# Kernel optimization log

Hardware: AMD Instinct MI355X
Metric: run time of the kernel (lower is better)

## Reference

```python
import jax, jax.numpy as jnp
import numpy as np

B = 64            # batch
C = 23            # chromosomes
E = 1024          # embedding_dim (eos)
D = 1024          # d_model
BOT = 128         # bottleneck_dim (embedding table width)
BINS = 8192       # bins per chromosome (num_bins_list entries)
NUM_BINS = C * BINS
S = 3             # num_states


def setup_inputs() -> dict:
    key = jax.random.key(0)
    ks = jax.random.split(key, 7)
    eos_emb = jax.random.normal(ks[0], (B, C, E), dtype=jnp.float32)
    # embedding table: indices used are 1..NUM_BINS (cum starts at 1), so NUM_BINS+2 rows
    emb_table = jax.random.normal(ks[1], (NUM_BINS + 2, BOT), dtype=jnp.float32) * 0.02
    Wb = jax.random.normal(ks[2], (D, BOT), dtype=jnp.float32) * 0.02   # bin_projection (no bias)
    We = jax.random.normal(ks[3], (D, E), dtype=jnp.float32) * 0.02     # eos_projection weight
    be = jax.random.normal(ks[4], (D,), dtype=jnp.float32) * 0.02       # eos_projection bias
    Wfc = jax.random.normal(ks[5], (S, 2 * D), dtype=jnp.float32) * 0.02  # fc weight
    bfc = jax.random.normal(ks[6], (S,), dtype=jnp.float32) * 0.02        # fc bias
    return {"eos_emb": eos_emb, "emb_table": emb_table, "Wb": Wb,
            "We": We, "be": be, "Wfc": Wfc, "bfc": bfc}


def reference(eos_emb, emb_table, Wb, We, be, Wfc, bfc):
    # eos_projection (use_eos_proj=True): [B, C, E] -> [B, C, D]
    eos = jnp.einsum('bce,de->bcd', eos_emb, We) + be
    # embedding lookup for all bins: indices 1..NUM_BINS (contiguous across chromosomes)
    idx = 1 + jnp.arange(NUM_BINS)
    # bin_projection (bottleneck_dim != d_model): [NUM_BINS, BOT] -> [NUM_BINS, D]
    bin_emb = jnp.einsum('nk,dk->nd', emb_table[idx], Wb).reshape(C, BINS, D)
    # fc on concat([bin_emb, eos]) == bin_emb @ W1^T + eos @ W2^T + b (avoids materializing concat)
    W1, W2 = Wfc[:, :D], Wfc[:, D:]
    part_bin = jnp.einsum('cnd,sd->cns', bin_emb, W1)   # [C, BINS, S]
    part_eos = jnp.einsum('bcd,sd->bcs', eos, W2)        # [B, C, S]
    # original returns list of 23 tensors [B, BINS, S]; stacked here as [B, C, BINS, S]
    out = jax.nn.relu(part_bin[None] + part_eos[:, :, None, :] + bfc)
    return out
```

## Files before the change

kernel.cpp:

```cpp
#include <hip/hip_runtime.h>

#define B_    64
#define C_    23
#define E_    1024
#define D_    1024
#define BOT_  128
#define BINS_ 8192
#define S_    3
#define NUMBINS (C_*BINS_)

typedef float f32x4 __attribute__((ext_vector_type(4)));

#define WS_M  0
#define WS_N  512
#define WS_C0 3584
#define WS_PE 3600

__global__ __launch_bounds__(256) void kprep(const float* __restrict__ Wb,
                                             const float* __restrict__ We,
                                             const float* __restrict__ be,
                                             const float* __restrict__ Wfc,
                                             const float* __restrict__ bfc,
                                             float* __restrict__ ws) {
    const int bx = blockIdx.x;
    const int t  = threadIdx.x;

    if (bx == 96 + 12) {
        int wave = t >> 6, lane = t & 63;
        if (wave < 3) {
            const float* w2 = Wfc + wave * 2 * D_ + D_;
            float acc = 0.f;
            #pragma unroll
            for (int j = 0; j < D_ / 64; j++) {
                int d = lane + j * 64;
                acc += w2[d] * be[d];
            }
            #pragma unroll
            for (int off = 32; off; off >>= 1) acc += __shfl_down(acc, off);
            if (lane == 0) ws[WS_C0 + wave] = acc + bfc[wave];
        }
        return;
    }

    __shared__ float wv[1024];
    __shared__ float red[256];

    const int og   = t & 31;
    const int dgrp = t >> 5;

    const float* src;
    const float* wrow;
    int ostride, obase;
    float* dst;

    if (bx < 96) {
        int s = bx >> 5, e0 = (bx & 31) * 32;
        src = We; ostride = E_; obase = e0;
        wrow = Wfc + s * 2 * D_ + D_;
        dst = ws + WS_N + s * E_ + e0;
    } else {
        int m = bx - 96;
        int s = m >> 2, k0 = (m & 3) * 32;
        src = Wb; ostride = BOT_; obase = k0;
        wrow = Wfc + s * 2 * D_;
        dst = ws + WS_M + s * BOT_ + k0;
    }

    for (int i = t; i < 1024; i += 256) wv[i] = wrow[i];
    __syncthreads();

    const float* p = src + (size_t)(dgrp * 128) * ostride + obase + og;
    const float* w = wv + dgrp * 128;
    float acc = 0.f;
    #pragma unroll 8
    for (int i = 0; i < 128; i++) {
        acc += w[i] * p[(size_t)i * ostride];
    }
    red[t] = acc;
    #pragma unroll
    for (int off = 128; off >= 32; off >>= 1) {
        __syncthreads();
        if (t < off) red[t] += red[t + off];
    }
    if (t < 32) dst[t] = red[t];
}

__global__ __launch_bounds__(256) void kpe(const float* __restrict__ eos,
                                           float* ws) {
    int wave = threadIdx.x >> 6;
    int lane = threadIdx.x & 63;
    int row  = blockIdx.x * 4 + wave;
    const float* x  = eos + (size_t)row * E_;
    const float* N0 = ws + WS_N;
    float a0 = 0.f, a1 = 0.f, a2 = 0.f;
    #pragma unroll
    for (int j = 0; j < E_ / 64; j++) {
        int i = lane + j * 64;
        float v = x[i];
        a0 += v * N0[i];
        a1 += v * N0[1024 + i];
        a2 += v * N0[2048 + i];
    }
    #pragma unroll
    for (int off = 32; off; off >>= 1) {
        a0 += __shfl_down(a0, off);
        a1 += __shfl_down(a1, off);
        a2 += __shfl_down(a2, off);
    }
    if (lane == 0) {
        float* pe = ws + WS_PE + row * 3;
        pe[0] = a0 + ws[WS_C0 + 0];
        pe[1] = a1 + ws[WS_C0 + 1];
        pe[2] = a2 + ws[WS_C0 + 2];
    }
}

__global__ __launch_bounds__(256) void kmain(const float* __restrict__ table,
                                             const float* __restrict__ ws,
                                             float* __restrict__ out) {
    const int t  = threadIdx.x;
    const int c  = blockIdx.y;
    const int n0 = blockIdx.x * 256;

    __shared__ float Ml[384];
    __shared__ float pbl[768];
    __shared__ float pel[192];

    for (int i = t; i < 384; i += 256) Ml[i] = ws[WS_M + i];
    if (t < 192) {
        int b = t / 3, s = t - b * 3;
        pel[t] = ws[WS_PE + (b * C_ + c) * 3 + s];
    }
    __syncthreads();

    const f32x4* row = (const f32x4*)(table + (size_t)(1 + c * BINS_ + n0 + t) * BOT_);
    float a0 = 0.f, a1 = 0.f, a2 = 0.f;
    #pragma unroll 8
    for (int k4 = 0; k4 < 32; k4++) {
        f32x4 v = row[k4];
        int k = k4 * 4;
        a0 += v.x * Ml[k]       + v.y * Ml[k + 1]   + v.z * Ml[k + 2]   + v.w * Ml[k + 3];
        a1 += v.x * Ml[128 + k] + v.y * Ml[129 + k] + v.z * Ml[130 + k] + v.w * Ml[131 + k];
        a2 += v.x * Ml[256 + k] + v.y * Ml[257 + k] + v.z * Ml[258 + k] + v.w * Ml[259 + k];
    }
    pbl[t * 3 + 0] = a0;
    pbl[t * 3 + 1] = a1;
    pbl[t * 3 + 2] = a2;
    __syncthreads();

    if (t < 192) {
        f32x4 pv = *(const f32x4*)&pbl[t * 4];
        int s0 = t % 3;
        int s1 = (s0 + 1 == 3) ? 0 : s0 + 1;
        int s2 = (s1 + 1 == 3) ? 0 : s1 + 1;
        for (int b = 0; b < B_; b++) {
            const float* pe = &pel[b * 3];
            f32x4 o;
            o.x = fmaxf(pv.x + pe[s0], 0.f);
            o.y = fmaxf(pv.y + pe[s1], 0.f);
            o.z = fmaxf(pv.z + pe[s2], 0.f);
            o.w = fmaxf(pv.w + pe[s0], 0.f);
            f32x4* dst = (f32x4*)(out + ((size_t)(b * C_ + c) * BINS_ + n0) * 3) + t;
            __builtin_nontemporal_store(o, dst);
        }
    }
}

extern "C" void kernel_launch(void* const* d_in, const int* in_sizes, int n_in,
                              void* d_out, int out_size, void* d_ws, size_t ws_size,
                              hipStream_t stream) {
    const float* eos   = (const float*)d_in[0];
    const float* table = (const float*)d_in[1];
    const float* Wb    = (const float*)d_in[2];
    const float* We    = (const float*)d_in[3];
    const float* be    = (const float*)d_in[4];
    const float* Wfc   = (const float*)d_in[5];
    const float* bfc   = (const float*)d_in[6];
    float* out = (float*)d_out;
    float* ws  = (float*)d_ws;

    kprep<<<109, 256, 0, stream>>>(Wb, We, be, Wfc, bfc, ws);
    kpe<<<368, 256, 0, stream>>>(eos, ws);
    dim3 g(32, 23);
    kmain<<<g, 256, 0, stream>>>(table, ws, out);
}
```

Measured before the change: 59.24 us.

## Restructure kernels: merge bin projection with eos dot, split output broadcast

The prep kernel now computes all three state rows per block, reading each We/Wb column once instead of three times, so it launches 37 blocks instead of 109. The bin-table projection moves into a middle kernel that also runs the per-(b,c) eos dot products in the same launch. The middle kernel parks part_bin in the batch-0 slice of the output, and a final kernel reads it back and broadcasts across the batch. This lets the heavy table read overlap the eos work, at the cost of an extra global round-trip for part_bin and a third launch that stays dependent.

```diff
diff --git a/kernel.cpp b/kernel.cpp
--- a/kernel.cpp
+++ b/kernel.cpp
@@ -25,7 +25,7 @@
     const int bx = blockIdx.x;
     const int t  = threadIdx.x;
 
-    if (bx == 96 + 12) {
+    if (bx == 36) {
         int wave = t >> 6, lane = t & 63;
         if (wave < 3) {
             const float* w2 = Wfc + wave * 2 * D_ + D_;
@@ -42,127 +42,150 @@
         return;
     }
 
-    __shared__ float wv[1024];
+    __shared__ float wv[3072];
     __shared__ float red[256];
 
     const int og   = t & 31;
     const int dgrp = t >> 5;
 
     const float* src;
-    const float* wrow;
-    int ostride, obase;
-    float* dst;
-
-    if (bx < 96) {
-        int s = bx >> 5, e0 = (bx & 31) * 32;
-        src = We; ostride = E_; obase = e0;
-        wrow = Wfc + s * 2 * D_ + D_;
-        dst = ws + WS_N + s * E_ + e0;
+    int ostride, obase, wofs;
+    float* dst0;
+    int dstride;
+
+    if (bx < 32) {
+        int e0 = bx * 32;
+        src = We; ostride = E_; obase = e0; wofs = D_;
+        dst0 = ws + WS_N + e0; dstride = E_;
     } else {
-        int m = bx - 96;
-        int s = m >> 2, k0 = (m & 3) * 32;
-        src = Wb; ostride = BOT_; obase = k0;
-        wrow = Wfc + s * 2 * D_;
-        dst = ws + WS_M + s * BOT_ + k0;
-    }
-
-    for (int i = t; i < 1024; i += 256) wv[i] = wrow[i];
+        int k0 = (bx - 32) * 32;
+        src = Wb; ostride = BOT_; obase = k0; wofs = 0;
+        dst0 = ws + WS_M + k0; dstride = BOT_;
+    }
+
+    for (int i = t; i < 3072; i += 256) {
+        int s = i >> 10, d = i & 1023;
+        wv[i] = Wfc[s * 2 * D_ + wofs + d];
+    }
     __syncthreads();
 
-    const float* p = src + (size_t)(dgrp * 128) * ostride + obase + og;
-    const float* w = wv + dgrp * 128;
-    float acc = 0.f;
+    const float* p  = src + (size_t)(dgrp * 128) * ostride + obase + og;
+    const float* w0 = wv + dgrp * 128;
+    float a0 = 0.f, a1 = 0.f, a2 = 0.f;
     #pragma unroll 8
     for (int i = 0; i < 128; i++) {
-        acc += w[i] * p[(size_t)i * ostride];
-    }
-    red[t] = acc;
-    #pragma unroll
-    for (int off = 128; off >= 32; off >>= 1) {
+        float v = p[(size_t)i * ostride];
+        a0 += w0[i] * v;
+        a1 += w0[1024 + i] * v;
+        a2 += w0[2048 + i] * v;
+    }
+    float accs[3] = {a0, a1, a2};
+    for (int s = 0; s < 3; s++) {
         __syncthreads();
-        if (t < off) red[t] += red[t + off];
-    }
-    if (t < 32) dst[t] = red[t];
-}
-
-__global__ __launch_bounds__(256) void kpe(const float* __restrict__ eos,
-                                           float* ws) {
-    int wave = threadIdx.x >> 6;
-    int lane = threadIdx.x & 63;
-    int row  = blockIdx.x * 4 + wave;
-    const float* x  = eos + (size_t)row * E_;
-    const float* N0 = ws + WS_N;
-    float a0 = 0.f, a1 = 0.f, a2 = 0.f;
-    #pragma unroll
-    for (int j = 0; j < E_ / 64; j++) {
-        int i = lane + j * 64;
-        float v = x[i];
-        a0 += v * N0[i];
-        a1 += v * N0[1024 + i];
-        a2 += v * N0[2048 + i];
-    }
-    #pragma unroll
-    for (int off = 32; off; off >>= 1) {
-        a0 += __shfl_down(a0, off);
-        a1 += __shfl_down(a1, off);
-        a2 += __shfl_down(a2, off);
-    }
-    if (lane == 0) {
-        float* pe = ws + WS_PE + row * 3;
-        pe[0] = a0 + ws[WS_C0 + 0];
-        pe[1] = a1 + ws[WS_C0 + 1];
-        pe[2] = a2 + ws[WS_C0 + 2];
-    }
-}
-
-__global__ __launch_bounds__(256) void kmain(const float* __restrict__ table,
-                                             const float* __restrict__ ws,
-                                             float* __restrict__ out) {
+        red[t] = accs[s];
+        #pragma unroll
+        for (int off = 128; off >= 32; off >>= 1) {
+            __syncthreads();
+            if (t < off) red[t] += red[t + off];
+        }
+        if (t < 32) dst0[s * dstride + t] = red[t];
+    }
+}
+
+__global__ __launch_bounds__(256) void kmid(const float* __restrict__ table,
+                                            const float* __restrict__ eos,
+                                            float* __restrict__ ws,
+                                            float* __restrict__ out) {
+    const int bx = blockIdx.x;
+    const int t  = threadIdx.x;
+
+    if (bx < 736) {
+        const int c  = bx >> 5;
+        const int n0 = (bx & 31) * 256;
+
+        __shared__ float Ml[384];
+        __shared__ float pbl[768];
+
+        for (int i = t; i < 384; i += 256) Ml[i] = ws[WS_M + i];
+        __syncthreads();
+
+        const f32x4* row = (const f32x4*)(table + (size_t)(1 + c * BINS_ + n0 + t) * BOT_);
+        float a0 = 0.f, a1 = 0.f, a2 = 0.f;
+        #pragma unroll 8
+        for (int k4 = 0; k4 < 32; k4++) {
+            f32x4 v = row[k4];
+            int k = k4 * 4;
+            a0 += v.x * Ml[k]       + v.y * Ml[k + 1]   + v.z * Ml[k + 2]   + v.w * Ml[k + 3];
+            a1 += v.x * Ml[128 + k] + v.y * Ml[129 + k] + v.z * Ml[130 + k] + v.w * Ml[131 + k];
+            a2 += v.x * Ml[256 + k] + v.y * Ml[257 + k] + v.z * Ml[258 + k] + v.w * Ml[259 + k];
+        }
+        pbl[t * 3 + 0] = a0;
+        pbl[t * 3 + 1] = a1;
+        pbl[t * 3 + 2] = a2;
+        __syncthreads();
+
+        if (t < 192) {
+            f32x4* dst = (f32x4*)(out + ((size_t)c * BINS_ + n0) * 3) + t;
+            *dst = *(const f32x4*)&pbl[t * 4];
+        }
+    } else {
+        int wave = t >> 6;
+        int lane = t & 63;
+        int row  = (bx - 736) * 4 + wave;
+        const float* x  = eos + (size_t)row * E_;
+        const float* N0 = ws + WS_N;
+        float a0 = 0.f, a1 = 0.f, a2 = 0.f;
+        #pragma unroll
+        for (int j = 0; j < E_ / 64; j++) {
+            int i = lane + j * 64;
+            float v = x[i];
+            a0 += v * N0[i];
+            a1 += v * N0[1024 + i];
+            a2 += v * N0[2048 + i];
+        }
+        #pragma unroll
+        for (int off = 32; off; off >>= 1) {
+            a0 += __shfl_down(a0, off);
+            a1 += __shfl_down(a1, off);
+            a2 += __shfl_down(a2, off);
+        }
+        if (lane == 0) {
+            float* pe = ws + WS_PE + row * 3;
+            pe[0] = a0 + ws[WS_C0 + 0];
+            pe[1] = a1 + ws[WS_C0 + 1];
+            pe[2] = a2 + ws[WS_C0 + 2];
+        }
+    }
+}
+
+__global__ __launch_bounds__(192) void kout(const float* __restrict__ ws,
+                                            float* __restrict__ out) {
     const int t  = threadIdx.x;
     const int c  = blockIdx.y;
     const int n0 = blockIdx.x * 256;
 
-    __shared__ float Ml[384];
-    __shared__ float pbl[768];
     __shared__ float pel[192];
 
-    for (int i = t; i < 384; i += 256) Ml[i] = ws[WS_M + i];
-    if (t < 192) {
+    f32x4 pv = *((const f32x4*)(out + ((size_t)c * BINS_ + n0) * 3) + t);
+
+    {
         int b = t / 3, s = t - b * 3;
         pel[t] = ws[WS_PE + (b * C_ + c) * 3 + s];
     }
     __syncthreads();
 
-    const f32x4* row = (const f32x4*)(table + (size_t)(1 + c * BINS_ + n0 + t) * BOT_);
-    float a0 = 0.f, a1 = 0.f, a2 = 0.f;
-    #pragma unroll 8
-    for (int k4 = 0; k4 < 32; k4++) {
-        f32x4 v = row[k4];
-        int k = k4 * 4;
-        a0 += v.x * Ml[k]       + v.y * Ml[k + 1]   + v.z * Ml[k + 2]   + v.w * Ml[k + 3];
-        a1 += v.x * Ml[128 + k] + v.y * Ml[129 + k] + v.z * Ml[130 + k] + v.w * Ml[131 + k];
-        a2 += v.x * Ml[256 + k] + v.y * Ml[257 + k] + v.z * Ml[258 + k] + v.w * Ml[259 + k];
-    }
-    pbl[t * 3 + 0] = a0;
-    pbl[t * 3 + 1] = a1;
-    pbl[t * 3 + 2] = a2;
-    __syncthreads();
-
-    if (t < 192) {
-        f32x4 pv = *(const f32x4*)&pbl[t * 4];
-        int s0 = t % 3;
-        int s1 = (s0 + 1 == 3) ? 0 : s0 + 1;
-        int s2 = (s1 + 1 == 3) ? 0 : s1 + 1;
-        for (int b = 0; b < B_; b++) {
-            const float* pe = &pel[b * 3];
-            f32x4 o;
-            o.x = fmaxf(pv.x + pe[s0], 0.f);
-            o.y = fmaxf(pv.y + pe[s1], 0.f);
-            o.z = fmaxf(pv.z + pe[s2], 0.f);
-            o.w = fmaxf(pv.w + pe[s0], 0.f);
-            f32x4* dst = (f32x4*)(out + ((size_t)(b * C_ + c) * BINS_ + n0) * 3) + t;
-            __builtin_nontemporal_store(o, dst);
-        }
+    int s0 = t % 3;
+    int s1 = (s0 + 1 == 3) ? 0 : s0 + 1;
+    int s2 = (s1 + 1 == 3) ? 0 : s1 + 1;
+    for (int b = 0; b < B_; b++) {
+        const float* pe = &pel[b * 3];
+        f32x4 o;
+        o.x = fmaxf(pv.x + pe[s0], 0.f);
+        o.y = fmaxf(pv.y + pe[s1], 0.f);
+        o.z = fmaxf(pv.z + pe[s2], 0.f);
+        o.w = fmaxf(pv.w + pe[s0], 0.f);
+        f32x4* dst = (f32x4*)(out + ((size_t)(b * C_ + c) * BINS_ + n0) * 3) + t;
+        __builtin_nontemporal_store(o, dst);
     }
 }
 
@@ -179,8 +202,8 @@
     float* out = (float*)d_out;
     float* ws  = (float*)d_ws;
 
-    kprep<<<109, 256, 0, stream>>>(Wb, We, be, Wfc, bfc, ws);
-    kpe<<<368, 256, 0, stream>>>(eos, ws);
+    kprep<<<37, 256, 0, stream>>>(Wb, We, be, Wfc, bfc, ws);
+    kmid<<<1104, 256, 0, stream>>>(table, eos, ws, out);
     dim3 g(32, 23);
-    kmain<<<g, 256, 0, stream>>>(table, ws, out);
-}
+    kout<<<g, 192, 0, stream>>>(ws, out);
+}
```

New measurement: 65.25 us. 1.1x slower.
